# Optimization experiments

Measured on AMD Instinct MI355X. Metric: run time of the kernel, lower is better.

## Reference

```python
import jax, jax.numpy as jnp
import numpy as np

N = 1024
V = 3889   # SMAL mesh vertices
NJ = 33    # kinematic-tree joints
NR = 35    # rotations in theta (35*3 = 105)
NB = 41    # shape betas
PARENTS = np.concatenate([[0], np.arange(NJ - 1)]).astype(np.int32)  # parent[i] < i
EXTRA_VERT_IDS = np.array([1863, 26, 2124, 150, 3055, 1097])


def _beta_scale_mask():
    m = np.zeros((NR, 3, 6), np.float32)
    leg = list(range(7, 15)) + list(range(17, 25))
    tail = list(range(25, 32))
    ears = [33, 34]
    m[leg, 2, 0] = 1.0; m[leg, 0, 1] = 1.0; m[leg, 1, 1] = 1.0
    m[tail, 0, 2] = 1.0; m[tail, 1, 3] = 1.0; m[tail, 2, 3] = 1.0
    m[ears, 1, 4] = 1.0; m[ears, 2, 5] = 1.0
    return jnp.asarray(m.reshape(NR * 3, 6).T)  # (6, 105)

BETA_SCALE_MASK = _beta_scale_mask()


def batch_rodrigues(theta):
    # theta: (M, 3) axis-angle -> (M, 3, 3) rotation matrices
    angle = jnp.linalg.norm(theta + 1e-8, axis=1, keepdims=True)  # (M,1)
    r = theta / angle
    c = jnp.cos(angle)[..., None]
    s = jnp.sin(angle)[..., None]
    outer = r[:, :, None] * r[:, None, :]
    z = jnp.zeros_like(r[:, 0])
    rx, ry, rz = r[:, 0], r[:, 1], r[:, 2]
    H = jnp.stack([z, -rz, ry, rz, z, -rx, -ry, rx, z], axis=1).reshape(-1, 3, 3)
    eye = jnp.eye(3, dtype=theta.dtype)
    return c * eye + (1.0 - c) * outer + s * H


def make_A(R, t):
    # R: (n,3,3), t: (n,3) -> homogeneous (n,4,4)
    top = jnp.concatenate([R, t[..., None]], axis=-1)
    bottom = jnp.broadcast_to(jnp.array([0.0, 0.0, 0.0, 1.0], dtype=R.dtype), (R.shape[0], 1, 4))
    return jnp.concatenate([top, bottom], axis=1)


def smal_forward(beta, theta, trans, betas_logscale, shapedirs, v_template, J_regressor, posedirs, weights):
    n = beta.shape[0]
    v_shaped = v_template + (beta @ shapedirs).reshape(n, V, 3)           # (n,V,3)
    J = jnp.einsum('nva,vj->nja', v_shaped, J_regressor)                  # (n,33,3)
    Rs = batch_rodrigues(theta.reshape(-1, 3)).reshape(n, NR, 3, 3)
    # pose blendshape term: original multiplies an all-zero pose_feature by posedirs
    v_posed = v_shaped + (jnp.zeros((1, 288), v_shaped.dtype) @ posedirs).reshape(1, V, 3)
    # per-joint anisotropic log-scales
    scal = jnp.exp(betas_logscale @ BETA_SCALE_MASK).reshape(n, NR, 3)    # (n,35,3)
    # kinematic chain (fixed 33-joint loop with parent dependency)
    results = [make_A(Rs[:, 0], J[:, 0])]
    for i in range(1, NJ):
        p = int(PARENTS[i])
        j_here = J[:, i] - J[:, p]
        # diag(1/s_parent) @ R @ diag(s_i), exact inverse of diagonal scale
        rot_new = Rs[:, i] * scal[:, i][:, None, :] / scal[:, p][:, :, None]
        results.append(results[p] @ make_A(rot_new, j_here))
    results = jnp.stack(results, axis=1)                                   # (n,33,4,4)
    init_bone = jnp.einsum('njxk,njk->njx', results[..., :3], J)           # (n,33,4)
    A = jnp.concatenate([results[..., :3], (results[..., 3] - init_bone)[..., None]], axis=-1)
    # linear blend skinning
    T = jnp.einsum('vj,njk->nvk', weights, A.reshape(n, NJ, 16)).reshape(n, V, 4, 4)
    v_homo = jnp.concatenate([v_posed * jnp.ones((n, 1, 1), v_posed.dtype),
                              jnp.ones((n, V, 1), v_posed.dtype)], axis=-1)
    verts = jnp.einsum('nvab,nvb->nva', T, v_homo)[..., :3] + trans[:, None, :]
    joints = jnp.einsum('nva,vj->nja', verts, J_regressor)                 # (n,33,3)
    joints = jnp.concatenate([joints, verts[:, EXTRA_VERT_IDS]], axis=1)   # (n,39,3)
    return verts, joints


def setup_inputs() -> dict:
    key = jax.random.key(0)
    ks = jax.random.split(key, 9)
    return {
        'beta': jax.random.normal(ks[0], (N, NB), jnp.float32) * 0.1,
        'theta': jax.random.normal(ks[1], (N, NR * 3), jnp.float32) * 0.2,
        'trans': jax.random.normal(ks[2], (N, 3), jnp.float32),
        'betas_logscale': jax.random.normal(ks[3], (N, 6), jnp.float32) * 0.1,
        'shapedirs': jax.random.normal(ks[4], (NB, V * 3), jnp.float32) * 0.01,
        'v_template': jax.random.normal(ks[5], (V, 3), jnp.float32),
        'J_regressor': jax.random.uniform(ks[6], (V, NJ), jnp.float32) / V,
        'posedirs': jax.random.normal(ks[7], (288, V * 3), jnp.float32) * 0.01,
        'weights': jax.random.uniform(ks[8], (V, NJ), jnp.float32),
    }


def reference(beta, theta, trans, betas_logscale, shapedirs, v_template, J_regressor, posedirs, weights):
    return smal_forward(beta, theta, trans, betas_logscale, shapedirs, v_template, J_regressor, posedirs, weights)
```

## Files before the change

kernel.cpp:

```cpp
#include <hip/hip_runtime.h>
#include <hip/hip_bf16.h>

#define NV 3889
#define NV3 11667
#define NVP 3904
#define NVAP 11712
#define NJC 33
#define NBB 41
#define NN 1024

__device__ const int EXTRA_IDS[6] = {1863, 26, 2124, 150, 3055, 1097};

#define WS_SJ    0
#define WS_WPK   4160
#define WS_SDPK  129088
#define WS_BPK   503872
#define WS_APK   536640
#define WS_JTL   929856
#define WS_JPART 1028160
#define WS_SJP   3387456

typedef __attribute__((ext_vector_type(8))) short short8v;
typedef __attribute__((ext_vector_type(4))) float f32x4;

__device__ __forceinline__ ushort bf16bits(float x) {
  __hip_bfloat16 h = __float2bfloat16(x);
  return *reinterpret_cast<ushort*>(&h);
}

#define PREP_PACK_BLOCKS 616
__global__ void __launch_bounds__(256) k_prep(
    const float* __restrict__ Jreg, const float* __restrict__ w,
    const float* __restrict__ beta, const float* __restrict__ sd,
    const float* __restrict__ vt, float* __restrict__ ws) {
  if (blockIdx.x < PREP_PACK_BLOCKS) {
    int id8 = blockIdx.x * 256 + threadIdx.x;
    const int R1 = NVP * 64 / 8;
    const int R2 = NVAP * 64 / 8;
    const int R3 = NN * 64 / 8;
    short8v pk;
    if (id8 < R1) {
      int u = id8 * 8;
      int v = u >> 6, j0 = u & 63;
#pragma unroll
      for (int e = 0; e < 8; e++) {
        int j = j0 + e;
        float val;
        if (j < NJC)      val = (v < NV) ? w[v * NJC + j] : 0.f;
        else if (j == 41) val = 1.f;
        else              val = 0.f;
        pk[e] = (short)bf16bits(val);
      }
      *(short8v*)((ushort*)(ws + WS_WPK) + u) = pk;
      return;
    }
    id8 -= R1;
    if (id8 < R2) {
      int u = id8 * 8;
      int va = u >> 6, bs0 = u & 63;
#pragma unroll
      for (int e = 0; e < 8; e++) {
        int bs = bs0 + e;
        float val = 0.f;
        if (va < NV3) {
          if (bs < NBB)       val = sd[(size_t)bs * NV3 + va];
          else if (bs == NBB) val = vt[va];
        }
        pk[e] = (short)bf16bits(val);
      }
      *(short8v*)((ushort*)(ws + WS_SDPK) + u) = pk;
      return;
    }
    id8 -= R2;
    if (id8 < R3) {
      int u = id8 * 8;
      int n = u >> 6, bs0 = u & 63;
#pragma unroll
      for (int e = 0; e < 8; e++) {
        int bs = bs0 + e;
        float val = (bs < NBB) ? beta[n * NBB + bs] : (bs == NBB ? 1.f : 0.f);
        pk[e] = (short)bf16bits(val);
      }
      *(short8v*)((ushort*)(ws + WS_BPK) + u) = pk;
      return;
    }
    id8 -= R3;
    {
      int u = id8 * 8;
      int tile = u >> 9, lane = (u >> 3) & 63;
      int jt = tile >> 7, kc = tile & 127;
      int j = jt * 16 + (lane & 15);
      int vb = kc * 32 + ((lane >> 4) << 3);
#pragma unroll
      for (int e = 0; e < 8; e++) {
        int v = vb + e;
        float val = (j < NJC && v < NV) ? Jreg[v * NJC + j] : 0.f;
        pk[e] = (short)bf16bits(val);
      }
      *(short8v*)((ushort*)(ws + WS_JTL) + u) = pk;
      return;
    }
  }
  int bid2 = blockIdx.x - PREP_PACK_BLOCKS;
  int b = bid2 >> 4, c = bid2 & 15;
  const float* src = (b < NBB) ? (sd + (size_t)b * NV3) : vt;
  int t = threadIdx.x;
  int dv = t / 33, j = t - dv * 33;
  float p0 = 0.f, p1 = 0.f, p2 = 0.f;
  int vbase = c * 244;
  int vend = vbase + 244;
  if (vend > NV) vend = NV;
  if (t < 231) {
    for (int v0 = vbase; v0 < vend; v0 += 7) {
      int v = v0 + dv;
      if (v < vend) {
        float jr = Jreg[v0 * 33 + t];
        p0 += src[v * 3 + 0] * jr;
        p1 += src[v * 3 + 1] * jr;
        p2 += src[v * 3 + 2] * jr;
      }
    }
  }
  __shared__ float sred[7][33][3];
  if (t < 231) { sred[dv][j][0] = p0; sred[dv][j][1] = p1; sred[dv][j][2] = p2; }
  __syncthreads();
  if (t < 99) {
    int jj = t / 3, aa = t - jj * 3;
    float s = 0.f;
#pragma unroll
    for (int d = 0; d < 7; d++) s += sred[d][jj][aa];
    ws[WS_SJP + bid2 * 100 + t] = s;
  }
}

__global__ void __launch_bounds__(256) k_sjr(float* __restrict__ ws) {
  int idx = blockIdx.x * 256 + threadIdx.x;
  if (idx >= 42 * 99) return;
  int b = idx / 99, k = idx - b * 99;
  float s = 0.f;
#pragma unroll
  for (int c = 0; c < 16; c++) s += ws[WS_SJP + (b * 16 + c) * 100 + k];
  ws[WS_SJ + idx] = s;
}

__device__ __forceinline__ void get_scal(int r, float e0, float e1, float e2, float e3,
                                         float s[3]) {
  bool leg  = (r >= 7 && r <= 14) || (r >= 17 && r <= 24);
  bool tail = (r >= 25 && r <= 31);
  s[0] = leg ? e1 : (tail ? e2 : 1.f);
  s[1] = leg ? e1 : (tail ? e3 : 1.f);
  s[2] = leg ? e0 : (tail ? e3 : 1.f);
}

__device__ __forceinline__ void rodrigues(const float* th, float R[9]) {
  float tx = th[0], ty = th[1], tz = th[2];
  float ax = tx + 1e-8f, ay = ty + 1e-8f, az = tz + 1e-8f;
  float angle = sqrtf(ax * ax + ay * ay + az * az);
  float inv = 1.f / angle;
  float rx = tx * inv, ry = ty * inv, rz = tz * inv;
  float c = cosf(angle), s = sinf(angle), o = 1.f - c;
  R[0] = c + o * rx * rx;      R[1] = o * rx * ry - s * rz; R[2] = o * rx * rz + s * ry;
  R[3] = o * rx * ry + s * rz; R[4] = c + o * ry * ry;      R[5] = o * ry * rz - s * rx;
  R[6] = o * rx * rz - s * ry; R[7] = o * ry * rz + s * rx; R[8] = c + o * rz * rz;
}

__global__ void __launch_bounds__(128) k_pose(
    const float* __restrict__ beta, const float* __restrict__ theta,
    const float* __restrict__ bls, const float* __restrict__ trans,
    float* __restrict__ ws) {
  int n = blockIdx.x, t = threadIdx.x;
  __shared__ float Jsh[99];
  __shared__ float Bsh[NJC * 12];
  __shared__ float Ash[NJC * 12];
  if (t < 99) {
    const float* SJ = ws + WS_SJ;
    float acc = SJ[NBB * 99 + t];
    const float* bn = beta + n * NBB;
#pragma unroll
    for (int b = 0; b < NBB; b++) acc += bn[b] * SJ[b * 99 + t];
    Jsh[t] = acc;
  }
  __syncthreads();
  if (t < NJC) {
    float R[9];
    rodrigues(theta + n * 105 + t * 3, R);
    float* B = Bsh + t * 12;
    if (t == 0) {
      B[0] = R[0]; B[1] = R[1]; B[2]  = R[2]; B[3]  = Jsh[0];
      B[4] = R[3]; B[5] = R[4]; B[6]  = R[5]; B[7]  = Jsh[1];
      B[8] = R[6]; B[9] = R[7]; B[10] = R[8]; B[11] = Jsh[2];
    } else {
      float e0 = expf(bls[n * 6 + 0]), e1 = expf(bls[n * 6 + 1]);
      float e2 = expf(bls[n * 6 + 2]), e3 = expf(bls[n * 6 + 3]);
      float si[3], sp[3];
      get_scal(t, e0, e1, e2, e3, si);
      get_scal(t - 1, e0, e1, e2, e3, sp);
#pragma unroll
      for (int r = 0; r < 3; r++) {
        float inv = 1.f / sp[r];
#pragma unroll
        for (int cc = 0; cc < 3; cc++) B[r * 4 + cc] = R[r * 3 + cc] * si[cc] * inv;
        B[r * 4 + 3] = Jsh[t * 3 + r] - Jsh[(t - 1) * 3 + r];
      }
    }
  }
  __syncthreads();
  if (t == 0) {
    float G[12];
#pragma unroll
    for (int k = 0; k < 12; k++) G[k] = Bsh[k];
#pragma unroll
    for (int i = 0; i < NJC; i++) {
      if (i > 0) {
        float b[12];
#pragma unroll
        for (int k = 0; k < 12; k++) b[k] = Bsh[i * 12 + k];
        float Gn[12];
#pragma unroll
        for (int r = 0; r < 3; r++) {
#pragma unroll
          for (int cc = 0; cc < 4; cc++) {
            float acc = G[r * 4 + 0] * b[0 * 4 + cc] + G[r * 4 + 1] * b[1 * 4 + cc] +
                        G[r * 4 + 2] * b[2 * 4 + cc];
            if (cc == 3) acc += G[r * 4 + 3];
            Gn[r * 4 + cc] = acc;
          }
        }
#pragma unroll
        for (int k = 0; k < 12; k++) G[k] = Gn[k];
      }
      float jx = Jsh[i * 3 + 0], jy = Jsh[i * 3 + 1], jz = Jsh[i * 3 + 2];
      float* Ai = Ash + i * 12;
      Ai[0] = G[0]; Ai[1] = G[1]; Ai[2]  = G[2];
      Ai[3] = G[3] - (G[0] * jx + G[1] * jy + G[2] * jz);
      Ai[4] = G[4]; Ai[5] = G[5]; Ai[6]  = G[6];
      Ai[7] = G[7] - (G[4] * jx + G[5] * jy + G[6] * jz);
      Ai[8] = G[8]; Ai[9] = G[9]; Ai[10] = G[10];
      Ai[11] = G[11] - (G[8] * jx + G[9] * jy + G[10] * jz);
    }
  }
  __syncthreads();
  __hip_bfloat16* apk = (__hip_bfloat16*)(ws + WS_APK) + (size_t)n * 768;
  for (int i = t; i < 768; i += 128) {
    int c = i >> 6, j = i & 63;
    float val = 0.f;
    if (j < NJC)                           val = Ash[j * 12 + c];
    else if (j == 41 && (c & 3) == 3)      val = trans[n * 3 + (c >> 2)];
    apk[i] = __float2bfloat16(val);
  }
}

#define ASH_USH (16 * 12 * 72)
#define VSL_USH (2 * 16 * 72)

__global__ void __launch_bounds__(512, 4) k_sv2(
    const float* __restrict__ ws, float* __restrict__ jpart,
    float* __restrict__ out, float* __restrict__ jout) {
  __shared__ __align__(16) ushort lds[ASH_USH + 8 * VSL_USH];
  int wv = threadIdx.x >> 6, lane = threadIdx.x & 63;
  int g = lane >> 4, c16 = lane & 15;
  int pg = blockIdx.x;
  int nc = blockIdx.y;
  int nb = nc * 16;
  const ushort* Wp = (const ushort*)(ws + WS_WPK);
  const ushort* Sp = (const ushort*)(ws + WS_SDPK);
  const ushort* Bp = (const ushort*)(ws + WS_BPK);
  const ushort* Ap = (const ushort*)(ws + WS_APK);
  const ushort* Jt = (const ushort*)(ws + WS_JTL);

  {
    const uint4* srcq = (const uint4*)(Ap + (size_t)nb * 768);
    for (int e = threadIdx.x; e < 1536; e += 512) {
      uint4 x = srcq[e];
      *(uint4*)(lds + (e >> 3) * 72 + (e & 7) * 8) = x;
    }
  }
  __syncthreads();

  ushort* vslA = lds + ASH_USH + wv * VSL_USH;
  ushort* vslB = vslA + 1152;
  bool act = g < 3;

  int p = pg * 8 + wv;
  bool pok = p < 122;

  f32x4 jc00, jc10, jc20, jc01, jc11, jc21, jc02, jc12, jc22;

  if (pok) {
    short8v bf0 = *(const short8v*)(Bp + (size_t)(nb + c16) * 64 + g * 8);
    short8v bf1 = *(const short8v*)(Bp + (size_t)(nb + c16) * 64 + 32 + g * 8);
    int vtA = p * 2, vtB = vtA + 1;
    int vA = vtA * 16 + c16, vB = vtB * 16 + c16;
    int vaA = vtA * 48 + c16, vaB = vtB * 48 + c16;
    {
      short8v s00 = *(const short8v*)(Sp + (size_t)(vaA +  0) * 64 + g * 8);
      short8v s01 = *(const short8v*)(Sp + (size_t)(vaA +  0) * 64 + 32 + g * 8);
      short8v s10 = *(const short8v*)(Sp + (size_t)(vaA + 16) * 64 + g * 8);
      short8v s11 = *(const short8v*)(Sp + (size_t)(vaA + 16) * 64 + 32 + g * 8);
      short8v s20 = *(const short8v*)(Sp + (size_t)(vaA + 32) * 64 + g * 8);
      short8v s21 = *(const short8v*)(Sp + (size_t)(vaA + 32) * 64 + 32 + g * 8);
      f32x4 a0 = {0,0,0,0}, a1 = {0,0,0,0}, a2 = {0,0,0,0};
      a0 = __builtin_amdgcn_mfma_f32_16x16x32_bf16(s00, bf0, a0, 0, 0, 0);
      a0 = __builtin_amdgcn_mfma_f32_16x16x32_bf16(s01, bf1, a0, 0, 0, 0);
      a1 = __builtin_amdgcn_mfma_f32_16x16x32_bf16(s10, bf0, a1, 0, 0, 0);
      a1 = __builtin_amdgcn_mfma_f32_16x16x32_bf16(s11, bf1, a1, 0, 0, 0);
      a2 = __builtin_amdgcn_mfma_f32_16x16x32_bf16(s20, bf0, a2, 0, 0, 0);
      a2 = __builtin_amdgcn_mfma_f32_16x16x32_bf16(s21, bf1, a2, 0, 0, 0);
      int wb = c16 * 72;
#pragma unroll
      for (int rr = 0; rr < 4; rr++) {
        int rho = g * 4 + rr;
        vslA[wb + (rho / 3) * 4 + (rho % 3)] = bf16bits(a0[rr]);
        rho = 16 + g * 4 + rr;
        vslA[wb + (rho / 3) * 4 + (rho % 3)] = bf16bits(a1[rr]);
        rho = 32 + g * 4 + rr;
        vslA[wb + (rho / 3) * 4 + (rho % 3)] = bf16bits(a2[rr]);
      }
    }
    {
      short8v s00 = *(const short8v*)(Sp + (size_t)(vaB +  0) * 64 + g * 8);
      short8v s01 = *(const short8v*)(Sp + (size_t)(vaB +  0) * 64 + 32 + g * 8);
      short8v s10 = *(const short8v*)(Sp + (size_t)(vaB + 16) * 64 + g * 8);
      short8v s11 = *(const short8v*)(Sp + (size_t)(vaB + 16) * 64 + 32 + g * 8);
      short8v s20 = *(const short8v*)(Sp + (size_t)(vaB + 32) * 64 + g * 8);
      short8v s21 = *(const short8v*)(Sp + (size_t)(vaB + 32) * 64 + 32 + g * 8);
      f32x4 a0 = {0,0,0,0}, a1 = {0,0,0,0}, a2 = {0,0,0,0};
      a0 = __builtin_amdgcn_mfma_f32_16x16x32_bf16(s00, bf0, a0, 0, 0, 0);
      a0 = __builtin_amdgcn_mfma_f32_16x16x32_bf16(s01, bf1, a0, 0, 0, 0);
      a1 = __builtin_amdgcn_mfma_f32_16x16x32_bf16(s10, bf0, a1, 0, 0, 0);
      a1 = __builtin_amdgcn_mfma_f32_16x16x32_bf16(s11, bf1, a1, 0, 0, 0);
      a2 = __builtin_amdgcn_mfma_f32_16x16x32_bf16(s20, bf0, a2, 0, 0, 0);
      a2 = __builtin_amdgcn_mfma_f32_16x16x32_bf16(s21, bf1, a2, 0, 0, 0);
      int wb = c16 * 72;
#pragma unroll
      for (int rr = 0; rr < 4; rr++) {
        int rho = g * 4 + rr;
        vslB[wb + (rho / 3) * 4 + (rho % 3)] = bf16bits(a0[rr]);
        rho = 16 + g * 4 + rr;
        vslB[wb + (rho / 3) * 4 + (rho % 3)] = bf16bits(a1[rr]);
        rho = 32 + g * 4 + rr;
        vslB[wb + (rho / 3) * 4 + (rho % 3)] = bf16bits(a2[rr]);
      }
    }
    short8v wfA0 = *(const short8v*)(Wp + (size_t)vA * 64 + g * 8);
    short8v wfA1 = *(const short8v*)(Wp + (size_t)vA * 64 + 32 + g * 8);
    short8v wfB0 = *(const short8v*)(Wp + (size_t)vB * 64 + g * 8);
    short8v wfB1 = *(const short8v*)(Wp + (size_t)vB * 64 + 32 + g * 8);
    int exA = -1, exB = -1;
#pragma unroll
    for (int e = 0; e < 6; e++) {
      if (vA == EXTRA_IDS[e]) exA = e;
      if (vB == EXTRA_IDS[e]) exB = e;
    }
#pragma unroll 4
    for (int np = 0; np < 16; np++) {
      const ushort* an = lds + np * 864 + c16 * 72 + g * 8;
      short8v af0 = *(const short8v*)(an);
      short8v af1 = *(const short8v*)(an + 32);
      f32x4 accA = {0,0,0,0}, accB = {0,0,0,0};
      accA = __builtin_amdgcn_mfma_f32_16x16x32_bf16(af0, wfA0, accA, 0, 0, 0);
      accA = __builtin_amdgcn_mfma_f32_16x16x32_bf16(af1, wfA1, accA, 0, 0, 0);
      accB = __builtin_amdgcn_mfma_f32_16x16x32_bf16(af0, wfB0, accB, 0, 0, 0);
      accB = __builtin_amdgcn_mfma_f32_16x16x32_bf16(af1, wfB1, accB, 0, 0, 0);
      uint2 qA = *(const uint2*)(vslA + np * 72 + c16 * 4);
      uint2 qB = *(const uint2*)(vslB + np * 72 + c16 * 4);
      float sxA = __uint_as_float((qA.x & 0xffffu) << 16);
      float syA = __uint_as_float(qA.x & 0xffff0000u);
      float szA = __uint_as_float((qA.y & 0xffffu) << 16);
      float sxB = __uint_as_float((qB.x & 0xffffu) << 16);
      float syB = __uint_as_float(qB.x & 0xffff0000u);
      float szB = __uint_as_float((qB.y & 0xffffu) << 16);
      float rA = fmaf(accA[0], sxA, fmaf(accA[1], syA, fmaf(accA[2], szA, accA[3])));
      float rB = fmaf(accB[0], sxB, fmaf(accB[1], syB, fmaf(accB[2], szB, accB[3])));
      if (act) {
        out[((size_t)(nb + np) * NV + vA) * 3 + g] = rA;
        if (vB < NV) out[((size_t)(nb + np) * NV + vB) * 3 + g] = rB;
        if (exA >= 0) jout[(size_t)(nb + np) * 117 + 99 + exA * 3 + g] = rA;
        if (exB >= 0) jout[(size_t)(nb + np) * 117 + 99 + exB * 3 + g] = rB;
        ushort* dst = (g < 2) ? (vslA + np * 72 + g * 32) : (vslB + np * 72);
        dst[c16]      = bf16bits(rA);
        dst[16 + c16] = bf16bits(rB);
      }
    }
    short8v ja0 = *(const short8v*)(Jt + ((size_t)(      p) << 9) + lane * 8);
    short8v ja1 = *(const short8v*)(Jt + ((size_t)(128 + p) << 9) + lane * 8);
    short8v ja2 = *(const short8v*)(Jt + ((size_t)(256 + p) << 9) + lane * 8);
    short8v vb0 = *(const short8v*)(vslA + c16 * 72 + g * 8);
    short8v vb1 = *(const short8v*)(vslA + c16 * 72 + 32 + g * 8);
    short8v vb2 = *(const short8v*)(vslB + c16 * 72 + g * 8);
    f32x4 z = {0, 0, 0, 0};
    jc00 = __builtin_amdgcn_mfma_f32_16x16x32_bf16(ja0, vb0, z, 0, 0, 0);
    jc10 = __builtin_amdgcn_mfma_f32_16x16x32_bf16(ja1, vb0, z, 0, 0, 0);
    jc20 = __builtin_amdgcn_mfma_f32_16x16x32_bf16(ja2, vb0, z, 0, 0, 0);
    jc01 = __builtin_amdgcn_mfma_f32_16x16x32_bf16(ja0, vb1, z, 0, 0, 0);
    jc11 = __builtin_amdgcn_mfma_f32_16x16x32_bf16(ja1, vb1, z, 0, 0, 0);
    jc21 = __builtin_amdgcn_mfma_f32_16x16x32_bf16(ja2, vb1, z, 0, 0, 0);
    jc02 = __builtin_amdgcn_mfma_f32_16x16x32_bf16(ja0, vb2, z, 0, 0, 0);
    jc12 = __builtin_amdgcn_mfma_f32_16x16x32_bf16(ja1, vb2, z, 0, 0, 0);
    jc22 = __builtin_amdgcn_mfma_f32_16x16x32_bf16(ja2, vb2, z, 0, 0, 0);
  } else {
    f32x4 z = {0, 0, 0, 0};
    jc00 = z; jc10 = z; jc20 = z;
    jc01 = z; jc11 = z; jc21 = z;
    jc02 = z; jc12 = z; jc22 = z;
  }

  __syncthreads();
  float* sc = (float*)lds;
  float* my = sc + (wv & 3) * 2304;
  int rb = (g * 4) * 16 + c16;
#define JST(JC, A, T) { float* q = my + ((A) * 3 + (T)) * 256 + rb; \
  q[0] = JC[0]; q[16] = JC[1]; q[32] = JC[2]; q[48] = JC[3]; }
#define JAC(JC, A, T) { float* q = my + ((A) * 3 + (T)) * 256 + rb; \
  q[0] += JC[0]; q[16] += JC[1]; q[32] += JC[2]; q[48] += JC[3]; }
  if (wv < 4) {
    JST(jc00, 0, 0) JST(jc10, 0, 1) JST(jc20, 0, 2)
    JST(jc01, 1, 0) JST(jc11, 1, 1) JST(jc21, 1, 2)
    JST(jc02, 2, 0) JST(jc12, 2, 1) JST(jc22, 2, 2)
  }
  __syncthreads();
  if (wv >= 4) {
    JAC(jc00, 0, 0) JAC(jc10, 0, 1) JAC(jc20, 0, 2)
    JAC(jc01, 1, 0) JAC(jc11, 1, 1) JAC(jc21, 1, 2)
    JAC(jc02, 2, 0) JAC(jc12, 2, 1) JAC(jc22, 2, 2)
  }
#undef JST
#undef JAC
  __syncthreads();
  float* jp = jpart + ((size_t)pg * 64 + nc) * 2304;
  for (int i = threadIdx.x; i < 2304; i += 512)
    jp[i] = sc[i] + sc[2304 + i] + sc[4608 + i] + sc[6912 + i];
}

__global__ void __launch_bounds__(256) k_jred(
    const float* __restrict__ jpart, float* __restrict__ jout) {
  int idx = blockIdx.x * 256 + threadIdx.x;
  if (idx >= NN * 99) return;
  int n = idx / 99, k = idx - n * 99;
  int j = k / 3, a = k - j * 3;
  int ncb = n >> 4, nl = n & 15;
  int jt = j >> 4, jl = j & 15;
  int ofs = ((a * 3 + jt) * 16 + jl) * 16 + nl;
  const float* base = jpart + (size_t)ncb * 2304 + ofs;
  float s = 0.f;
#pragma unroll
  for (int pgi = 0; pgi < 16; pgi++) s += base[(size_t)pgi * 64 * 2304];
  jout[(size_t)n * 117 + j * 3 + a] = s;
}

extern "C" void kernel_launch(void* const* d_in, const int* in_sizes, int n_in,
                              void* d_out, int out_size, void* d_ws, size_t ws_size,
                              hipStream_t stream) {
  const float* beta       = (const float*)d_in[0];
  const float* theta      = (const float*)d_in[1];
  const float* trans      = (const float*)d_in[2];
  const float* bls        = (const float*)d_in[3];
  const float* shapedirs  = (const float*)d_in[4];
  const float* v_template = (const float*)d_in[5];
  const float* Jreg       = (const float*)d_in[6];
  const float* weights    = (const float*)d_in[8];
  float* out = (float*)d_out;
  float* ws  = (float*)d_ws;
  float* jout = out + (size_t)NN * NV3;
  float* jpart = ws + WS_JPART;

  k_prep<<<PREP_PACK_BLOCKS + 672, 256, 0, stream>>>(Jreg, weights, beta,
                                                     shapedirs, v_template, ws);
  k_sjr<<<17, 256, 0, stream>>>(ws);
  k_pose<<<NN, 128, 0, stream>>>(beta, theta, bls, trans, ws);
  dim3 gsv(16, 64);
  k_sv2<<<gsv, 512, 0, stream>>>(ws, jpart, out, jout);
  k_jred<<<(NN * 99 + 255) / 256, 256, 0, stream>>>(jpart, jout);
}
```

Baseline: 79.80 us.

## Replace joint partial buffer and reduction kernel with atomics; transpose shapedirs via LDS

Result: slower. 92.36 us (+15.7%).

```diff
diff --git a/kernel.cpp b/kernel.cpp
--- a/kernel.cpp
+++ b/kernel.cpp
@@ -17,8 +17,7 @@
 #define WS_BPK   503872
 #define WS_APK   536640
 #define WS_JTL   929856
-#define WS_JPART 1028160
-#define WS_SJP   3387456
+#define WS_SJP   1028160
 
 typedef __attribute__((ext_vector_type(8))) short short8v;
 typedef __attribute__((ext_vector_type(4))) float f32x4;
@@ -28,15 +27,75 @@
   return *reinterpret_cast<ushort*>(&h);
 }
 
-#define PREP_PACK_BLOCKS 616
+#define PREP_SJ_BLOCKS 672
+#define PREP_SD_BLOCKS 366
+#define PREP_PK_BLOCKS 250
+#define PREP_Z_BLOCKS  117
 __global__ void __launch_bounds__(256) k_prep(
     const float* __restrict__ Jreg, const float* __restrict__ w,
     const float* __restrict__ beta, const float* __restrict__ sd,
-    const float* __restrict__ vt, float* __restrict__ ws) {
-  if (blockIdx.x < PREP_PACK_BLOCKS) {
-    int id8 = blockIdx.x * 256 + threadIdx.x;
+    const float* __restrict__ vt, float* __restrict__ ws,
+    float* __restrict__ jout) {
+  int bx = blockIdx.x;
+  int t = threadIdx.x;
+  if (bx < PREP_SJ_BLOCKS) {
+    int bid2 = bx;
+    int b = bid2 >> 4, c = bid2 & 15;
+    const float* src = (b < NBB) ? (sd + (size_t)b * NV3) : vt;
+    int dv = t / 33, j = t - dv * 33;
+    float p0 = 0.f, p1 = 0.f, p2 = 0.f;
+    int vbase = c * 244;
+    int vend = vbase + 244;
+    if (vend > NV) vend = NV;
+    if (t < 231) {
+      for (int v0 = vbase; v0 < vend; v0 += 7) {
+        int v = v0 + dv;
+        if (v < vend) {
+          float jr = Jreg[v0 * 33 + t];
+          p0 += src[v * 3 + 0] * jr;
+          p1 += src[v * 3 + 1] * jr;
+          p2 += src[v * 3 + 2] * jr;
+        }
+      }
+    }
+    __shared__ float sred[7][33][3];
+    if (t < 231) { sred[dv][j][0] = p0; sred[dv][j][1] = p1; sred[dv][j][2] = p2; }
+    __syncthreads();
+    if (t < 99) {
+      int jj = t / 3, aa = t - jj * 3;
+      float s = 0.f;
+#pragma unroll
+      for (int d = 0; d < 7; d++) s += sred[d][jj][aa];
+      ws[WS_SJP + bid2 * 100 + t] = s;
+    }
+    return;
+  }
+  bx -= PREP_SJ_BLOCKS;
+  if (bx < PREP_SD_BLOCKS) {
+    __shared__ ushort tl[32 * 50];
+    int va0 = bx * 32;
+    for (int i = t; i < 42 * 32; i += 256) {
+      int bs = i >> 5, off = i & 31;
+      int va = va0 + off;
+      float v = 0.f;
+      if (va < NV3) v = (bs < NBB) ? sd[(size_t)bs * NV3 + va] : vt[va];
+      tl[off * 50 + bs] = bf16bits(v);
+    }
+    __syncthreads();
+    int va_l = t >> 3, ch = t & 7;
+    short8v pk;
+#pragma unroll
+    for (int e = 0; e < 8; e++) {
+      int bs = ch * 8 + e;
+      pk[e] = (bs < 42) ? (short)tl[va_l * 50 + bs] : (short)0;
+    }
+    *(short8v*)((ushort*)(ws + WS_SDPK) + ((size_t)(va0 + va_l) * 64 + ch * 8)) = pk;
+    return;
+  }
+  bx -= PREP_SD_BLOCKS;
+  if (bx < PREP_PK_BLOCKS) {
+    int id8 = bx * 256 + t;
     const int R1 = NVP * 64 / 8;
-    const int R2 = NVAP * 64 / 8;
     const int R3 = NN * 64 / 8;
     short8v pk;
     if (id8 < R1) {
@@ -55,23 +114,6 @@
       return;
     }
     id8 -= R1;
-    if (id8 < R2) {
-      int u = id8 * 8;
-      int va = u >> 6, bs0 = u & 63;
-#pragma unroll
-      for (int e = 0; e < 8; e++) {
-        int bs = bs0 + e;
-        float val = 0.f;
-        if (va < NV3) {
-          if (bs < NBB)       val = sd[(size_t)bs * NV3 + va];
-          else if (bs == NBB) val = vt[va];
-        }
-        pk[e] = (short)bf16bits(val);
-      }
-      *(short8v*)((ushort*)(ws + WS_SDPK) + u) = pk;
-      return;
-    }
-    id8 -= R2;
     if (id8 < R3) {
       int u = id8 * 8;
       int n = u >> 6, bs0 = u & 63;
@@ -101,35 +143,11 @@
       return;
     }
   }
-  int bid2 = blockIdx.x - PREP_PACK_BLOCKS;
-  int b = bid2 >> 4, c = bid2 & 15;
-  const float* src = (b < NBB) ? (sd + (size_t)b * NV3) : vt;
-  int t = threadIdx.x;
-  int dv = t / 33, j = t - dv * 33;
-  float p0 = 0.f, p1 = 0.f, p2 = 0.f;
-  int vbase = c * 244;
-  int vend = vbase + 244;
-  if (vend > NV) vend = NV;
-  if (t < 231) {
-    for (int v0 = vbase; v0 < vend; v0 += 7) {
-      int v = v0 + dv;
-      if (v < vend) {
-        float jr = Jreg[v0 * 33 + t];
-        p0 += src[v * 3 + 0] * jr;
-        p1 += src[v * 3 + 1] * jr;
-        p2 += src[v * 3 + 2] * jr;
-      }
-    }
-  }
-  __shared__ float sred[7][33][3];
-  if (t < 231) { sred[dv][j][0] = p0; sred[dv][j][1] = p1; sred[dv][j][2] = p2; }
-  __syncthreads();
-  if (t < 99) {
-    int jj = t / 3, aa = t - jj * 3;
-    float s = 0.f;
-#pragma unroll
-    for (int d = 0; d < 7; d++) s += sred[d][jj][aa];
-    ws[WS_SJP + bid2 * 100 + t] = s;
+  bx -= PREP_PK_BLOCKS;
+  {
+    int idx = bx * 256 + t;
+    f32x4 z = {0.f, 0.f, 0.f, 0.f};
+    ((f32x4*)jout)[idx] = z;
   }
 }
 
@@ -254,8 +272,8 @@
 #define VSL_USH (2 * 16 * 72)
 
 __global__ void __launch_bounds__(512, 4) k_sv2(
-    const float* __restrict__ ws, float* __restrict__ jpart,
-    float* __restrict__ out, float* __restrict__ jout) {
+    const float* __restrict__ ws, float* __restrict__ out,
+    float* __restrict__ jout) {
   __shared__ __align__(16) ushort lds[ASH_USH + 8 * VSL_USH];
   int wv = threadIdx.x >> 6, lane = threadIdx.x & 63;
   int g = lane >> 4, c16 = lane & 15;
@@ -427,25 +445,15 @@
 #undef JST
 #undef JAC
   __syncthreads();
-  float* jp = jpart + ((size_t)pg * 64 + nc) * 2304;
-  for (int i = threadIdx.x; i < 2304; i += 512)
-    jp[i] = sc[i] + sc[2304 + i] + sc[4608 + i] + sc[6912 + i];
-}
-
-__global__ void __launch_bounds__(256) k_jred(
-    const float* __restrict__ jpart, float* __restrict__ jout) {
-  int idx = blockIdx.x * 256 + threadIdx.x;
-  if (idx >= NN * 99) return;
-  int n = idx / 99, k = idx - n * 99;
-  int j = k / 3, a = k - j * 3;
-  int ncb = n >> 4, nl = n & 15;
-  int jt = j >> 4, jl = j & 15;
-  int ofs = ((a * 3 + jt) * 16 + jl) * 16 + nl;
-  const float* base = jpart + (size_t)ncb * 2304 + ofs;
-  float s = 0.f;
-#pragma unroll
-  for (int pgi = 0; pgi < 16; pgi++) s += base[(size_t)pgi * 64 * 2304];
-  jout[(size_t)n * 117 + j * 3 + a] = s;
+  for (int i = threadIdx.x; i < 2304; i += 512) {
+    float val = sc[i] + sc[2304 + i] + sc[4608 + i] + sc[6912 + i];
+    int ra = i >> 8;
+    int aa = ra / 3, jt2 = ra - aa * 3;
+    int jl = (i >> 4) & 15, nl = i & 15;
+    int j = jt2 * 16 + jl;
+    if (j < NJC)
+      atomicAdd(jout + (size_t)(nb + nl) * 117 + j * 3 + aa, val);
+  }
 }
 
 extern "C" void kernel_launch(void* const* d_in, const int* in_sizes, int n_in,
@@ -462,13 +470,11 @@
   float* out = (float*)d_out;
   float* ws  = (float*)d_ws;
   float* jout = out + (size_t)NN * NV3;
-  float* jpart = ws + WS_JPART;
-
-  k_prep<<<PREP_PACK_BLOCKS + 672, 256, 0, stream>>>(Jreg, weights, beta,
-                                                     shapedirs, v_template, ws);
+
+  k_prep<<<PREP_SJ_BLOCKS + PREP_SD_BLOCKS + PREP_PK_BLOCKS + PREP_Z_BLOCKS,
+           256, 0, stream>>>(Jreg, weights, beta, shapedirs, v_template, ws, jout);
   k_sjr<<<17, 256, 0, stream>>>(ws);
   k_pose<<<NN, 128, 0, stream>>>(beta, theta, bls, trans, ws);
   dim3 gsv(16, 64);
-  k_sv2<<<gsv, 512, 0, stream>>>(ws, jpart, out, jout);
-  k_jred<<<(NN * 99 + 255) / 256, 256, 0, stream>>>(jpart, jout);
-}
+  k_sv2<<<gsv, 512, 0, stream>>>(ws, out, jout);
+}
```

## Transpose shapedirs via LDS in prep and read skinning matrices from global

Applied to the files above, without the earlier changes.

Measured after the change: 97.20 us. +21.8%, slower.

```diff
diff --git a/kernel.cpp b/kernel.cpp
--- a/kernel.cpp
+++ b/kernel.cpp
@@ -17,8 +17,8 @@
 #define WS_BPK   503872
 #define WS_APK   536640
 #define WS_JTL   929856
-#define WS_JPART 1028160
-#define WS_SJP   3387456
+#define WS_SJP   1028160
+#define WS_JPART 1095360
 
 typedef __attribute__((ext_vector_type(8))) short short8v;
 typedef __attribute__((ext_vector_type(4))) float f32x4;
@@ -28,15 +28,73 @@
   return *reinterpret_cast<ushort*>(&h);
 }
 
-#define PREP_PACK_BLOCKS 616
+#define PREP_SJ_BLOCKS 672
+#define PREP_SD_BLOCKS 366
+#define PREP_PK_BLOCKS 250
 __global__ void __launch_bounds__(256) k_prep(
     const float* __restrict__ Jreg, const float* __restrict__ w,
     const float* __restrict__ beta, const float* __restrict__ sd,
     const float* __restrict__ vt, float* __restrict__ ws) {
-  if (blockIdx.x < PREP_PACK_BLOCKS) {
-    int id8 = blockIdx.x * 256 + threadIdx.x;
+  int bx = blockIdx.x;
+  int t = threadIdx.x;
+  if (bx < PREP_SJ_BLOCKS) {
+    int bid2 = bx;
+    int b = bid2 >> 4, c = bid2 & 15;
+    const float* src = (b < NBB) ? (sd + (size_t)b * NV3) : vt;
+    int dv = t / 33, j = t - dv * 33;
+    float p0 = 0.f, p1 = 0.f, p2 = 0.f;
+    int vbase = c * 244;
+    int vend = vbase + 244;
+    if (vend > NV) vend = NV;
+    if (t < 231) {
+      for (int v0 = vbase; v0 < vend; v0 += 7) {
+        int v = v0 + dv;
+        if (v < vend) {
+          float jr = Jreg[v0 * 33 + t];
+          p0 += src[v * 3 + 0] * jr;
+          p1 += src[v * 3 + 1] * jr;
+          p2 += src[v * 3 + 2] * jr;
+        }
+      }
+    }
+    __shared__ float sred[7][33][3];
+    if (t < 231) { sred[dv][j][0] = p0; sred[dv][j][1] = p1; sred[dv][j][2] = p2; }
+    __syncthreads();
+    if (t < 99) {
+      int jj = t / 3, aa = t - jj * 3;
+      float s = 0.f;
+#pragma unroll
+      for (int d = 0; d < 7; d++) s += sred[d][jj][aa];
+      ws[WS_SJP + bid2 * 100 + t] = s;
+    }
+    return;
+  }
+  bx -= PREP_SJ_BLOCKS;
+  if (bx < PREP_SD_BLOCKS) {
+    __shared__ ushort tl[32 * 50];
+    int va0 = bx * 32;
+    for (int i = t; i < 42 * 32; i += 256) {
+      int bs = i >> 5, off = i & 31;
+      int va = va0 + off;
+      float v = 0.f;
+      if (va < NV3) v = (bs < NBB) ? sd[(size_t)bs * NV3 + va] : vt[va];
+      tl[off * 50 + bs] = bf16bits(v);
+    }
+    __syncthreads();
+    int va_l = t >> 3, ch = t & 7;
+    short8v pk;
+#pragma unroll
+    for (int e = 0; e < 8; e++) {
+      int bs = ch * 8 + e;
+      pk[e] = (bs < 42) ? (short)tl[va_l * 50 + bs] : (short)0;
+    }
+    *(short8v*)((ushort*)(ws + WS_SDPK) + ((size_t)(va0 + va_l) * 64 + ch * 8)) = pk;
+    return;
+  }
+  bx -= PREP_SD_BLOCKS;
+  {
+    int id8 = bx * 256 + t;
     const int R1 = NVP * 64 / 8;
-    const int R2 = NVAP * 64 / 8;
     const int R3 = NN * 64 / 8;
     short8v pk;
     if (id8 < R1) {
@@ -55,23 +113,6 @@
       return;
     }
     id8 -= R1;
-    if (id8 < R2) {
-      int u = id8 * 8;
-      int va = u >> 6, bs0 = u & 63;
-#pragma unroll
-      for (int e = 0; e < 8; e++) {
-        int bs = bs0 + e;
-        float val = 0.f;
-        if (va < NV3) {
-          if (bs < NBB)       val = sd[(size_t)bs * NV3 + va];
-          else if (bs == NBB) val = vt[va];
-        }
-        pk[e] = (short)bf16bits(val);
-      }
-      *(short8v*)((ushort*)(ws + WS_SDPK) + u) = pk;
-      return;
-    }
-    id8 -= R2;
     if (id8 < R3) {
       int u = id8 * 8;
       int n = u >> 6, bs0 = u & 63;
@@ -100,36 +141,6 @@
       *(short8v*)((ushort*)(ws + WS_JTL) + u) = pk;
       return;
     }
-  }
-  int bid2 = blockIdx.x - PREP_PACK_BLOCKS;
-  int b = bid2 >> 4, c = bid2 & 15;
-  const float* src = (b < NBB) ? (sd + (size_t)b * NV3) : vt;
-  int t = threadIdx.x;
-  int dv = t / 33, j = t - dv * 33;
-  float p0 = 0.f, p1 = 0.f, p2 = 0.f;
-  int vbase = c * 244;
-  int vend = vbase + 244;
-  if (vend > NV) vend = NV;
-  if (t < 231) {
-    for (int v0 = vbase; v0 < vend; v0 += 7) {
-      int v = v0 + dv;
-      if (v < vend) {
-        float jr = Jreg[v0 * 33 + t];
-        p0 += src[v * 3 + 0] * jr;
-        p1 += src[v * 3 + 1] * jr;
-        p2 += src[v * 3 + 2] * jr;
-      }
-    }
-  }
-  __shared__ float sred[7][33][3];
-  if (t < 231) { sred[dv][j][0] = p0; sred[dv][j][1] = p1; sred[dv][j][2] = p2; }
-  __syncthreads();
-  if (t < 99) {
-    int jj = t / 3, aa = t - jj * 3;
-    float s = 0.f;
-#pragma unroll
-    for (int d = 0; d < 7; d++) s += sred[d][jj][aa];
-    ws[WS_SJP + bid2 * 100 + t] = s;
   }
 }
 
@@ -250,13 +261,12 @@
   }
 }
 
-#define ASH_USH (16 * 12 * 72)
 #define VSL_USH (2 * 16 * 72)
 
 __global__ void __launch_bounds__(512, 4) k_sv2(
     const float* __restrict__ ws, float* __restrict__ jpart,
     float* __restrict__ out, float* __restrict__ jout) {
-  __shared__ __align__(16) ushort lds[ASH_USH + 8 * VSL_USH];
+  __shared__ __align__(16) ushort lds[8 * VSL_USH];
   int wv = threadIdx.x >> 6, lane = threadIdx.x & 63;
   int g = lane >> 4, c16 = lane & 15;
   int pg = blockIdx.x;
@@ -268,16 +278,7 @@
   const ushort* Ap = (const ushort*)(ws + WS_APK);
   const ushort* Jt = (const ushort*)(ws + WS_JTL);
 
-  {
-    const uint4* srcq = (const uint4*)(Ap + (size_t)nb * 768);
-    for (int e = threadIdx.x; e < 1536; e += 512) {
-      uint4 x = srcq[e];
-      *(uint4*)(lds + (e >> 3) * 72 + (e & 7) * 8) = x;
-    }
-  }
-  __syncthreads();
-
-  ushort* vslA = lds + ASH_USH + wv * VSL_USH;
+  ushort* vslA = lds + wv * VSL_USH;
   ushort* vslB = vslA + 1152;
   bool act = g < 3;
 
@@ -352,9 +353,10 @@
       if (vA == EXTRA_IDS[e]) exA = e;
       if (vB == EXTRA_IDS[e]) exB = e;
     }
+    const ushort* anb = Ap + (size_t)nb * 768 + c16 * 64 + g * 8;
 #pragma unroll 4
     for (int np = 0; np < 16; np++) {
-      const ushort* an = lds + np * 864 + c16 * 72 + g * 8;
+      const ushort* an = anb + np * 768;
       short8v af0 = *(const short8v*)(an);
       short8v af1 = *(const short8v*)(an + 32);
       f32x4 accA = {0,0,0,0}, accB = {0,0,0,0};
@@ -464,8 +466,8 @@
   float* jout = out + (size_t)NN * NV3;
   float* jpart = ws + WS_JPART;
 
-  k_prep<<<PREP_PACK_BLOCKS + 672, 256, 0, stream>>>(Jreg, weights, beta,
-                                                     shapedirs, v_template, ws);
+  k_prep<<<PREP_SJ_BLOCKS + PREP_SD_BLOCKS + PREP_PK_BLOCKS, 256, 0, stream>>>(
+      Jreg, weights, beta, shapedirs, v_template, ws);
   k_sjr<<<17, 256, 0, stream>>>(ws);
   k_pose<<<NN, 128, 0, stream>>>(beta, theta, bls, trans, ws);
   dim3 gsv(16, 64);
```
